# Kernel tuning notes

Hardware: AMD Instinct MI355X
Metric: run time of the kernel (lower is better)

The kernel has to match this reference:

```python
import jax, jax.numpy as jnp
import numpy as np

B, K, D = 8192, 64, 128
LOW_BOUND = 1
TAU = 1.0  # global_step=None -> tau = 1.0


def setup_inputs() -> dict:
    key = jax.random.key(0)
    ks = jax.random.split(key, 7)
    slots = jax.random.normal(ks[0], (B, K, D), dtype=jnp.float32)
    gumbel_u = jax.random.uniform(ks[1], (B, K, 2), dtype=jnp.float32)
    fix_u = jax.random.uniform(ks[2], (B, K), dtype=jnp.float32)
    # score_net params: Linear(D, D//2) -> ReLU -> Linear(D//2, 2)
    H = D // 2
    W1 = jax.random.normal(ks[3], (D, H), dtype=jnp.float32) / np.sqrt(D)
    b1 = jnp.zeros((H,), dtype=jnp.float32)
    W2 = jax.random.normal(ks[4], (H, 2), dtype=jnp.float32) / np.sqrt(H)
    b2 = jnp.zeros((2,), dtype=jnp.float32)
    return {"slots": slots, "gumbel_u": gumbel_u, "fix_u": fix_u,
            "W1": W1, "b1": b1, "W2": W2, "b2": b2}


def reference(slots, gumbel_u, fix_u, W1, b1, W2, b2):
    # score_net MLP: [B,K,D] -> [B,K,2]
    h = jax.nn.relu(jnp.einsum('bkd,dh->bkh', slots, W1) + b1)
    logits = jnp.einsum('bkh,ht->bkt', h, W2) + b2

    # hard gumbel-softmax (training path), straight-through estimator
    u = jnp.clip(gumbel_u, 1e-10, 1.0 - 1e-7)
    g = -jnp.log(-jnp.log(u))
    y_soft = jax.nn.softmax((logits + g) / TAU, axis=-1)
    y_hard = jax.nn.one_hot(jnp.argmax(y_soft, axis=-1), 2, dtype=y_soft.dtype)
    y = y_hard + y_soft - jax.lax.stop_gradient(y_soft)
    decision = y[..., 1]  # [B, K]

    # vectorized _ensure_minimum_slots: activate `deficit` random inactive slots
    active = decision != 0                                   # [B, K]
    needed = jnp.maximum(LOW_BOUND - active.sum(-1), 0)[:, None]  # [B, 1]
    keys = jnp.where(active, -jnp.inf, fix_u)                # random keys on inactive slots
    ranks = jnp.argsort(jnp.argsort(-keys, axis=-1), axis=-1)  # rank 0 = largest key
    activate = (ranks < needed) & (~active)
    decision = jnp.where(activate, jnp.asarray(1.0, decision.dtype), decision)

    keep_probs = jax.nn.softmax(logits, axis=-1)[..., 1]     # [B, K]
    return decision, keep_probs
```

## Files before the change

### kernel.cpp

```cpp
#include <hip/hip_runtime.h>


constexpr int D = 128;
constexpr int H = 64;
constexpr int NROWS = 8192 * 64;

__global__ __launch_bounds__(256, 4)
void gumbel_slot_kernel(const float* __restrict__ slots,
                        const float* __restrict__ gumbel_u,
                        const float* __restrict__ fix_u,
                        const float* __restrict__ W1,
                        const float* __restrict__ b1,
                        const float* __restrict__ W2,
                        const float* __restrict__ b2,
                        float* __restrict__ out)
{
    __shared__ float s_lds[256 * 36];
    const int tid = threadIdx.x;
    const int r0  = blockIdx.x * 256;
    const int r   = r0 + tid;

    float acc[H];
#pragma unroll
    for (int j = 0; j < H; ++j) acc[j] = b1[j];

#pragma unroll 1
    for (int c = 0; c < 4; ++c) {
#pragma unroll
        for (int i = 0; i < 8; ++i) {
            const int linear = (i << 8) + tid;
            const int row    = linear >> 3;
            const int col4   = (linear & 7) << 2;
            const float4 v = *reinterpret_cast<const float4*>(
                slots + (size_t)(r0 + row) * D + (c << 5) + col4);
            *reinterpret_cast<float4*>(&s_lds[row * 36 + col4]) = v;
        }
        __syncthreads();
        const float* __restrict__ wbase = W1 + (c << 5) * H;
#pragma unroll 1
        for (int d4 = 0; d4 < 8; ++d4) {
            const float4 s4 =
                *reinterpret_cast<const float4*>(&s_lds[tid * 36 + (d4 << 2)]);
            const float sv[4] = {s4.x, s4.y, s4.z, s4.w};
#pragma unroll
            for (int dd = 0; dd < 4; ++dd) {
                const float s = sv[dd];
                const float* __restrict__ w = wbase + ((d4 << 2) + dd) * H;
#pragma unroll
                for (int j = 0; j < H; ++j) acc[j] = fmaf(s, w[j], acc[j]);
            }
        }
        __syncthreads();
    }

    float l0 = b2[0], l1 = b2[1];
#pragma unroll
    for (int j = 0; j < H; ++j) {
        const float h = fmaxf(acc[j], 0.0f);
        l0 = fmaf(h, W2[2 * j + 0], l0);
        l1 = fmaf(h, W2[2 * j + 1], l1);
    }

    const float2 u2 = *reinterpret_cast<const float2*>(gumbel_u + (size_t)r * 2);
    const float lo = 1e-10f, hi = (float)(1.0 - 1e-7);
    const float u0 = fminf(fmaxf(u2.x, lo), hi);
    const float u1 = fminf(fmaxf(u2.y, lo), hi);
    const float g0 = -logf(-logf(u0));
    const float g1 = -logf(-logf(u1));
    const float z0 = l0 + g0, z1 = l1 + g1;
    float dec = (z1 > z0) ? 1.0f : 0.0f;

    const float m  = fmaxf(l0, l1);
    const float e0 = expf(l0 - m), e1 = expf(l1 - m);
    const float keep = e1 / (e0 + e1);

    const unsigned long long act = __ballot(dec != 0.0f);
    if (act == 0ull) {
        const int lane = tid & 63;
        float v   = fix_u[r];
        int   idx = lane;
#pragma unroll
        for (int off = 32; off > 0; off >>= 1) {
            const float ov   = __shfl_xor(v, off, 64);
            const int   oidx = __shfl_xor(idx, off, 64);
            if (ov > v || (ov == v && oidx < idx)) { v = ov; idx = oidx; }
        }
        if (lane == idx) dec = 1.0f;
    }

    out[r] = dec;
    out[NROWS + r] = keep;
}

extern "C" void kernel_launch(void* const* d_in, const int* in_sizes, int n_in,
                              void* d_out, int out_size, void* d_ws, size_t ws_size,
                              hipStream_t stream)
{
    const float* slots  = (const float*)d_in[0];
    const float* gumbel = (const float*)d_in[1];
    const float* fixu   = (const float*)d_in[2];
    const float* W1     = (const float*)d_in[3];
    const float* b1     = (const float*)d_in[4];
    const float* W2     = (const float*)d_in[5];
    const float* b2     = (const float*)d_in[6];
    float* out = (float*)d_out;

    gumbel_slot_kernel<<<NROWS / 256, 256, 0, stream>>>(
        slots, gumbel, fixu, W1, b1, W2, b2, out);
}
```

Before: 450.1 us.

## Replace scalar FP32 MLP with split-bf16 MFMA emulation and persistent tiles

Rewrites the first MLP layer to use bf16 MFMA instructions, emulating FP32 precision by splitting each operand into three bf16 parts and accumulating six cross products. W1 is split once per block into a swizzled LDS layout, and the grid becomes 512 persistent blocks of 512 threads, each handling two 512-row tiles. The second layer is reduced through a shared-memory transpose with block barriers. The aim is to move the dominant FMA work off the scalar ALUs onto matrix units, at the cost of extra split arithmetic and a result that is close to, but not exactly, FP32.

```diff
diff --git a/kernel.cpp b/kernel.cpp
--- a/kernel.cpp
+++ b/kernel.cpp
@@ -1,95 +1,179 @@
 #include <hip/hip_runtime.h>
 
 
-constexpr int D = 128;
-constexpr int H = 64;
+typedef __attribute__((ext_vector_type(8))) short bf16x8;
+typedef __attribute__((ext_vector_type(4))) float f32x4;
+
 constexpr int NROWS = 8192 * 64;
+constexpr int D = 128, H = 64;
 
-__global__ __launch_bounds__(256, 4)
-void gumbel_slot_kernel(const float* __restrict__ slots,
-                        const float* __restrict__ gumbel_u,
-                        const float* __restrict__ fix_u,
-                        const float* __restrict__ W1,
-                        const float* __restrict__ b1,
-                        const float* __restrict__ W2,
-                        const float* __restrict__ b2,
-                        float* __restrict__ out)
+__device__ __forceinline__ void split3(float x, unsigned& h1, unsigned& h2, unsigned& h3) {
+    unsigned ux = __float_as_uint(x);
+    h1 = ux & 0xFFFF0000u;
+    float r = x - __uint_as_float(h1);
+    h2 = __float_as_uint(r) & 0xFFFF0000u;
+    float r2 = r - __uint_as_float(h2);
+    h3 = __float_as_uint(r2) & 0xFFFF0000u;
+}
+
+__global__ __launch_bounds__(512, 2)
+void gumbel_slot_mfma(const float* __restrict__ slots,
+                      const float* __restrict__ gumbel_u,
+                      const float* __restrict__ fix_u,
+                      const float* __restrict__ W1,
+                      const float* __restrict__ b1,
+                      const float* __restrict__ W2,
+                      const float* __restrict__ b2,
+                      float* __restrict__ out)
 {
-    __shared__ float s_lds[256 * 36];
-    const int tid = threadIdx.x;
-    const int r0  = blockIdx.x * 256;
-    const int r   = r0 + tid;
+    __shared__ __align__(16) unsigned short wt[3 * 64 * 128];
+    __shared__ __align__(16) float red[8][16][16][2];
 
-    float acc[H];
+    const int tid  = threadIdx.x;
+    const int wv   = tid >> 6;
+    const int lane = tid & 63;
+    const int quad = lane >> 4;
+    const int col  = lane & 15;
+
 #pragma unroll
-    for (int j = 0; j < H; ++j) acc[j] = b1[j];
+    for (int i = 0; i < 16; ++i) {
+        const int e = i * 512 + tid;
+        const int d = e >> 6, j = e & 63;
+        unsigned h1, h2, h3;
+        split3(W1[e], h1, h2, h3);
+        const int chunk = (d >> 3) ^ (j & 15);
+        const int idx = j * 128 + chunk * 8 + (d & 7);
+        wt[idx]             = (unsigned short)(h1 >> 16);
+        wt[idx + 8192]      = (unsigned short)(h2 >> 16);
+        wt[idx + 16384]     = (unsigned short)(h3 >> 16);
+    }
+    __syncthreads();
+
+    float  b1v[4];
+    float2 w2v[4];
+#pragma unroll
+    for (int nt = 0; nt < 4; ++nt) {
+        b1v[nt] = b1[nt * 16 + col];
+        w2v[nt] = *(const float2*)(W2 + (size_t)(nt * 16 + col) * 2);
+    }
+    const float2 b2v = *(const float2*)b2;
 
 #pragma unroll 1
-    for (int c = 0; c < 4; ++c) {
+    for (int t = 0; t < 2; ++t) {
+        const int tile = blockIdx.x + t * 512;
+        const int rowW = tile * 512 + wv * 64;
+        const int r    = rowW + lane;
+
+        f32x4 acc[4][4];
 #pragma unroll
-        for (int i = 0; i < 8; ++i) {
-            const int linear = (i << 8) + tid;
-            const int row    = linear >> 3;
-            const int col4   = (linear & 7) << 2;
-            const float4 v = *reinterpret_cast<const float4*>(
-                slots + (size_t)(r0 + row) * D + (c << 5) + col4);
-            *reinterpret_cast<float4*>(&s_lds[row * 36 + col4]) = v;
-        }
-        __syncthreads();
-        const float* __restrict__ wbase = W1 + (c << 5) * H;
+        for (int mt = 0; mt < 4; ++mt)
+#pragma unroll
+            for (int nt = 0; nt < 4; ++nt)
+                acc[mt][nt] = f32x4{b1v[nt], b1v[nt], b1v[nt], b1v[nt]};
+
 #pragma unroll 1
-        for (int d4 = 0; d4 < 8; ++d4) {
-            const float4 s4 =
-                *reinterpret_cast<const float4*>(&s_lds[tid * 36 + (d4 << 2)]);
-            const float sv[4] = {s4.x, s4.y, s4.z, s4.w};
+        for (int ks = 0; ks < 4; ++ks) {
+            bf16x8 a1[4], a2[4], a3[4];
 #pragma unroll
-            for (int dd = 0; dd < 4; ++dd) {
-                const float s = sv[dd];
-                const float* __restrict__ w = wbase + ((d4 << 2) + dd) * H;
+            for (int mt = 0; mt < 4; ++mt) {
+                const float* arow = slots + (size_t)(rowW + mt * 16 + col) * D
+                                          + ks * 32 + quad * 8;
+                const float4 x0 = *(const float4*)arow;
+                const float4 x1 = *(const float4*)(arow + 4);
+                const float xs[8] = {x0.x, x0.y, x0.z, x0.w, x1.x, x1.y, x1.z, x1.w};
+                union { int i[4]; bf16x8 v; } u1, u2, u3;
 #pragma unroll
-                for (int j = 0; j < H; ++j) acc[j] = fmaf(s, w[j], acc[j]);
+                for (int p = 0; p < 4; ++p) {
+                    unsigned xh1, xh2, xh3, yh1, yh2, yh3;
+                    split3(xs[2 * p],     xh1, xh2, xh3);
+                    split3(xs[2 * p + 1], yh1, yh2, yh3);
+                    u1.i[p] = (int)((xh1 >> 16) | yh1);
+                    u2.i[p] = (int)((xh2 >> 16) | yh2);
+                    u3.i[p] = (int)((xh3 >> 16) | yh3);
+                }
+                a1[mt] = u1.v; a2[mt] = u2.v; a3[mt] = u3.v;
+            }
+#pragma unroll
+            for (int nt = 0; nt < 4; ++nt) {
+                const int j = nt * 16 + col;
+                const int chunk = (ks * 4 + quad) ^ col;
+                const unsigned short* wp = &wt[j * 128 + chunk * 8];
+                const bf16x8 bq1 = *(const bf16x8*)(wp);
+                const bf16x8 bq2 = *(const bf16x8*)(wp + 8192);
+                const bf16x8 bq3 = *(const bf16x8*)(wp + 16384);
+#pragma unroll
+                for (int mt = 0; mt < 4; ++mt) {
+                    f32x4 c = acc[mt][nt];
+                    c = __builtin_amdgcn_mfma_f32_16x16x32_bf16(a1[mt], bq1, c, 0, 0, 0);
+                    c = __builtin_amdgcn_mfma_f32_16x16x32_bf16(a2[mt], bq1, c, 0, 0, 0);
+                    c = __builtin_amdgcn_mfma_f32_16x16x32_bf16(a1[mt], bq2, c, 0, 0, 0);
+                    c = __builtin_amdgcn_mfma_f32_16x16x32_bf16(a2[mt], bq2, c, 0, 0, 0);
+                    c = __builtin_amdgcn_mfma_f32_16x16x32_bf16(a1[mt], bq3, c, 0, 0, 0);
+                    c = __builtin_amdgcn_mfma_f32_16x16x32_bf16(a3[mt], bq1, c, 0, 0, 0);
+                    acc[mt][nt] = c;
+                }
             }
         }
-        __syncthreads();
+
+        float fl0 = 0.f, fl1 = 0.f;
+#pragma unroll 1
+        for (int mt = 0; mt < 4; ++mt) {
+#pragma unroll
+            for (int reg = 0; reg < 4; ++reg) {
+                float p0 = 0.f, p1 = 0.f;
+#pragma unroll
+                for (int nt = 0; nt < 4; ++nt) {
+                    const float h = fmaxf(acc[mt][nt][reg], 0.f);
+                    p0 = fmaf(h, w2v[nt].x, p0);
+                    p1 = fmaf(h, w2v[nt].y, p1);
+                }
+                const int rl = quad * 4 + reg;
+                *(float2*)&red[wv][rl][col ^ rl][0] = make_float2(p0, p1);
+            }
+            __syncthreads();
+            if ((lane >> 4) == mt) {
+                const int rl = col;
+                float s0 = 0.f, s1 = 0.f;
+#pragma unroll
+                for (int c = 0; c < 16; ++c) {
+                    const float2 v = *(const float2*)&red[wv][rl][c ^ rl][0];
+                    s0 += v.x; s1 += v.y;
+                }
+                fl0 = s0; fl1 = s1;
+            }
+            __syncthreads();
+        }
+        const float l0 = fl0 + b2v.x;
+        const float l1 = fl1 + b2v.y;
+
+        const float2 u2 = *(const float2*)(gumbel_u + (size_t)r * 2);
+        const float lo = 1e-10f, hi = (float)(1.0 - 1e-7);
+        const float u0 = fminf(fmaxf(u2.x, lo), hi);
+        const float u1 = fminf(fmaxf(u2.y, lo), hi);
+        const float g0 = -logf(-logf(u0));
+        const float g1 = -logf(-logf(u1));
+        float dec = ((l1 + g1) > (l0 + g0)) ? 1.0f : 0.0f;
+
+        const float m  = fmaxf(l0, l1);
+        const float e0 = expf(l0 - m), e1 = expf(l1 - m);
+        const float keep = e1 / (e0 + e1);
+
+        const unsigned long long act = __ballot(dec != 0.0f);
+        if (act == 0ull) {
+            float v = fix_u[r];
+            int  idx = lane;
+#pragma unroll
+            for (int off = 32; off > 0; off >>= 1) {
+                const float ov  = __shfl_xor(v, off, 64);
+                const int  oidx = __shfl_xor(idx, off, 64);
+                if (ov > v || (ov == v && oidx < idx)) { v = ov; idx = oidx; }
+            }
+            if (lane == idx) dec = 1.0f;
+        }
+
+        out[r] = dec;
+        out[NROWS + r] = keep;
     }
-
-    float l0 = b2[0], l1 = b2[1];
-#pragma unroll
-    for (int j = 0; j < H; ++j) {
-        const float h = fmaxf(acc[j], 0.0f);
-        l0 = fmaf(h, W2[2 * j + 0], l0);
-        l1 = fmaf(h, W2[2 * j + 1], l1);
-    }
-
-    const float2 u2 = *reinterpret_cast<const float2*>(gumbel_u + (size_t)r * 2);
-    const float lo = 1e-10f, hi = (float)(1.0 - 1e-7);
-    const float u0 = fminf(fmaxf(u2.x, lo), hi);
-    const float u1 = fminf(fmaxf(u2.y, lo), hi);
-    const float g0 = -logf(-logf(u0));
-    const float g1 = -logf(-logf(u1));
-    const float z0 = l0 + g0, z1 = l1 + g1;
-    float dec = (z1 > z0) ? 1.0f : 0.0f;
-
-    const float m  = fmaxf(l0, l1);
-    const float e0 = expf(l0 - m), e1 = expf(l1 - m);
-    const float keep = e1 / (e0 + e1);
-
-    const unsigned long long act = __ballot(dec != 0.0f);
-    if (act == 0ull) {
-        const int lane = tid & 63;
-        float v   = fix_u[r];
-        int   idx = lane;
-#pragma unroll
-        for (int off = 32; off > 0; off >>= 1) {
-            const float ov   = __shfl_xor(v, off, 64);
-            const int   oidx = __shfl_xor(idx, off, 64);
-            if (ov > v || (ov == v && oidx < idx)) { v = ov; idx = oidx; }
-        }
-        if (lane == idx) dec = 1.0f;
-    }
-
-    out[r] = dec;
-    out[NROWS + r] = keep;
 }
 
 extern "C" void kernel_launch(void* const* d_in, const int* in_sizes, int n_in,
@@ -105,6 +189,6 @@
     const float* b2     = (const float*)d_in[6];
     float* out = (float*)d_out;
 
-    gumbel_slot_kernel<<<NROWS / 256, 256, 0, stream>>>(
+    gumbel_slot_mfma<<<512, 512, 0, stream>>>(
         slots, gumbel, fixu, W1, b1, W2, b2, out);
 }
```

New measurement: 419.3 us. 6.9% less time.
